# Optimization experiments

Hardware: AMD Instinct MI355X
Metric: run time of the kernel (lower is better)

## Reference

```python
import jax, jax.numpy as jnp
import numpy as np

B, N_CHANS, T = 128, 64, 1000
SPATIAL_EXP, SPATIAL_MERGE = 240, 32
FILTERS = [41, 51, 61]
TEMP_EXP = 2
BASE = 2
FEATURE_DIM = [(SPATIAL_EXP // (N_CHANS - BASE**i + 1), BASE**i)
               for i in range(2, 6) if BASE**i < N_CHANS] + [(SPATIAL_EXP, N_CHANS)]
SUM_SP = sum(d0 * (N_CHANS - d1 + 1) for d0, d1 in FEATURE_DIM)   # 1078
N_FEAT = len(FILTERS) * TEMP_EXP * SPATIAL_MERGE                  # 192
FC_IN = (N_FEAT + 1) * N_FEAT // 2                                # 18528
N_CLASS = 4
BN_EPS = 1e-5


def _conv2d(x, w, b, groups=1, pad_w=0):
    y = jax.lax.conv_general_dilated(
        x, w, (1, 1), ((0, 0), (pad_w, pad_w)),
        dimension_numbers=('NCHW', 'OIHW', 'NCHW'),
        feature_group_count=groups)
    return y + b[None, :, None, None]


def _bn(x, gamma, beta):
    # inference-mode BatchNorm2d with running_mean=0, running_var=1
    return gamma[None, :, None, None] * x * (1.0 / np.sqrt(1.0 + BN_EPS)) + beta[None, :, None, None]


def setup_inputs() -> dict:
    key = jax.random.key(0)
    ks = iter(jax.random.split(key, 40))
    inp = {"x": jax.random.normal(next(ks), (B, N_CHANS, T), jnp.float32)}
    for i, (d0, d1) in enumerate(FEATURE_DIM):
        inp[f"sw{i}"] = jax.random.normal(next(ks), (d0, 1, d1, 1), jnp.float32) / np.sqrt(d1)
        inp[f"sb{i}"] = jnp.zeros((d0,), jnp.float32)
    inp["mw"] = jax.random.normal(next(ks), (SPATIAL_MERGE, 1, SUM_SP, 1), jnp.float32) / np.sqrt(SUM_SP)
    inp["mb"] = jnp.zeros((SPATIAL_MERGE,), jnp.float32)
    inp["mg"] = jnp.ones((SPATIAL_MERGE,), jnp.float32)
    inp["mbt"] = jnp.zeros((SPATIAL_MERGE,), jnp.float32)
    for i, size in enumerate(FILTERS):
        co = TEMP_EXP * SPATIAL_MERGE
        inp[f"tw{i}"] = jax.random.normal(next(ks), (co, 1, 1, size), jnp.float32) / np.sqrt(size)
        inp[f"tb{i}"] = jnp.zeros((co,), jnp.float32)
        inp[f"tg{i}"] = jnp.ones((co,), jnp.float32)
        inp[f"tbt{i}"] = jnp.zeros((co,), jnp.float32)
    inp["fcw"] = jax.random.normal(next(ks), (N_CLASS, FC_IN), jnp.float32) / np.sqrt(FC_IN)
    inp["fcb"] = jnp.zeros((N_CLASS,), jnp.float32)
    return inp


def reference(x, sw0, sb0, sw1, sb1, sw2, sb2, sw3, sb3, sw4, sb4,
              mw, mb, mg, mbt,
              tw0, tb0, tg0, tbt0, tw1, tb1, tg1, tbt1, tw2, tb2, tg2, tbt2,
              fcw, fcb):
    b, _, t = x.shape
    xi = x[:, None]                                        # (B,1,C,T)
    sp = [(sw0, sb0), (sw1, sb1), (sw2, sb2), (sw3, sb3), (sw4, sb4)]
    feats = [_conv2d(xi, w, bb).reshape(b, -1, t) for w, bb in sp]
    Xs = jnp.concatenate(feats, 1)[:, None]                # (B,1,1078,T)
    Xs = _bn(_conv2d(Xs, mw, mb), mg, mbt)                 # (B,32,1,T)
    tp = [(tw0, tb0, tg0, tbt0), (tw1, tb1, tg1, tbt1), (tw2, tb2, tg2, tbt2)]
    Xt = jnp.stack([_bn(_conv2d(Xs, w, bb, groups=SPATIAL_MERGE, pad_w=w.shape[-1] // 2), g, bt)
                    for w, bb, g, bt in tp], 1)            # (B,3,64,1,T)
    Xt = Xt.reshape(b, -1, t)                              # (B,192,T)
    Xb = jnp.einsum('bct,bdt->bcd', Xt, Xt) / (t - 1)      # Gram matrix (B,192,192)
    L = jnp.linalg.cholesky(Xb)
    n = L.shape[-1]
    rows, cols = np.tril_indices(n, -1)                    # row-major: matches torch per-row concat
    diag = jnp.diagonal(L, axis1=1, axis2=2)               # (B,192)
    tangent = jnp.concatenate([jnp.log(diag), L[:, rows, cols]], axis=1)  # (B,18528)
    return tangent @ fcw.T + fcb
```

## Files before the change

### kernel.cpp

```cpp
#include <hip/hip_runtime.h>
#include <hip/hip_bf16.h>
#include <math.h>


#define A_OFF    0
#define BETA_OFF 2048
#define TBE_OFF  2080
#define TWE_OFF  2304
#define XS_OFF   14592
#define XBP_OFF  4110592
#define XT_OFF   7256320
#define WS_NEED  ((size_t)19839232 * 4)

#define SBN 0.9999950000374997f

typedef short short8 __attribute__((ext_vector_type(8)));
typedef float floatx4 __attribute__((ext_vector_type(4)));

__device__ __forceinline__ unsigned short f2bf(float f) {
    unsigned u = __float_as_uint(f);
    u += 0x7FFFu + ((u >> 16) & 1u);
    return (unsigned short)(u >> 16);
}
__device__ __forceinline__ float bf2f(unsigned short h) {
    return __uint_as_float(((unsigned)h) << 16);
}

__global__ __launch_bounds__(256) void prep_kernel(
    const float* __restrict__ sw0, const float* __restrict__ sw1,
    const float* __restrict__ sw2, const float* __restrict__ sw3,
    const float* __restrict__ sw4,
    const float* __restrict__ sb0, const float* __restrict__ sb1,
    const float* __restrict__ sb2, const float* __restrict__ sb3,
    const float* __restrict__ sb4,
    const float* __restrict__ mw, const float* __restrict__ mb,
    const float* __restrict__ mg, const float* __restrict__ mbt,
    const float* __restrict__ tw0, const float* __restrict__ tw1,
    const float* __restrict__ tw2,
    const float* __restrict__ tb0, const float* __restrict__ tb1,
    const float* __restrict__ tb2,
    const float* __restrict__ tg0, const float* __restrict__ tg1,
    const float* __restrict__ tg2,
    const float* __restrict__ tbt0, const float* __restrict__ tbt1,
    const float* __restrict__ tbt2,
    float* __restrict__ ws)
{
    const float* tws[3]  = {tw0, tw1, tw2};
    const float* tbs[3]  = {tb0, tb1, tb2};
    const float* tgs[3]  = {tg0, tg1, tg2};
    const float* tbts[3] = {tbt0, tbt1, tbt2};
    const int fsz[3] = {41, 51, 61};

    int gid = blockIdx.x * 256 + threadIdx.x;
    int gw = gid >> 6, lane = gid & 63;

    if (gw < 2048) {
        int m = gw >> 6, c = gw & 63;
        float acc = 0.f;
        for (int j = lane; j < 1078; j += 64) {
            float wv = mw[m * 1078 + j];
            float sv = 0.f;
            if (j < 183) {
                int r = j, fq = r / 61, h = r - fq * 61, k = c - h;
                if (k >= 0 && k < 4)  sv = sw0[fq * 4 + k];
            } else if (j < 411) {
                int r = j - 183, fq = r / 57, h = r - fq * 57, k = c - h;
                if (k >= 0 && k < 8)  sv = sw1[fq * 8 + k];
            } else if (j < 607) {
                int r = j - 411, fq = r / 49, h = r - fq * 49, k = c - h;
                if (k >= 0 && k < 16) sv = sw2[fq * 16 + k];
            } else if (j < 838) {
                int r = j - 607, fq = r / 33, h = r - fq * 33, k = c - h;
                if (k >= 0 && k < 32) sv = sw3[fq * 32 + k];
            } else {
                int r = j - 838;
                sv = sw4[r * 64 + c];
            }
            acc += wv * sv;
        }
        for (int off = 32; off > 0; off >>= 1) acc += __shfl_down(acc, off);
        if (lane == 0) ws[A_OFF + m * 64 + c] = mg[m] * SBN * acc;
    } else if (gw < 2080) {
        int m = gw - 2048;
        float acc = 0.f;
        for (int j = lane; j < 1078; j += 64) {
            float wv = mw[m * 1078 + j];
            float sv;
            if (j < 183)      sv = sb0[j / 61];
            else if (j < 411) sv = sb1[(j - 183) / 57];
            else if (j < 607) sv = sb2[(j - 411) / 49];
            else if (j < 838) sv = sb3[(j - 607) / 33];
            else              sv = sb4[j - 838];
            acc += wv * sv;
        }
        for (int off = 32; off > 0; off >>= 1) acc += __shfl_down(acc, off);
        if (lane == 0)
            ws[BETA_OFF + m] = mg[m] * SBN * (acc + mb[m]) + mbt[m];
    } else {
        int id2 = gid - 133120;
        if (id2 < 0) return;
        if (id2 < 192) {
            int fi = id2 >> 6, o = id2 & 63;
            ws[TBE_OFF + id2] = tgs[fi][o] * SBN * tbs[fi][o] + tbts[fi][o];
        } else if (id2 < 12480) {
            int idx = id2 - 192;
            int fi = idx >> 12, r = idx & 4095, o = r >> 6, k = r & 63;
            int sz = fsz[fi];
            float v = 0.f;
            if (k < sz) v = tgs[fi][o] * SBN * tws[fi][o * sz + k];
            ws[TWE_OFF + idx] = v;
        }
    }
}

__global__ __launch_bounds__(256) void xs_kernel(const float* __restrict__ x,
                                                 float* __restrict__ ws)
{
    __shared__ float Ash[2048];
    __shared__ float Bsh[32];
    int tid = threadIdx.x;
    for (int i = tid; i < 2048; i += 256) Ash[i] = ws[A_OFF + i];
    if (tid < 32) Bsh[tid] = ws[BETA_OFF + tid];
    __syncthreads();

    int gid = blockIdx.x * 256 + tid;
    int b = gid / 1000, t = gid - b * 1000;
    const float* xp = x + b * 64000 + t;

    float acc[32];
#pragma unroll
    for (int m = 0; m < 32; ++m) acc[m] = Bsh[m];
#pragma unroll 4
    for (int c = 0; c < 64; ++c) {
        float xv = xp[c * 1000];
#pragma unroll
        for (int m = 0; m < 32; ++m) acc[m] += Ash[m * 64 + c] * xv;
    }
    float* op = ws + XS_OFF + b * 32000 + t;
#pragma unroll
    for (int m = 0; m < 32; ++m) op[m * 1000] = acc[m];
}

__device__ __forceinline__ void conv8_vals(float* __restrict__ a,
                                           const float* __restrict__ xp,
                                           const unsigned short* __restrict__ wp,
                                           int szp, float bias)
{
    float xw[8];
#pragma unroll
    for (int i = 0; i < 8; ++i) { a[i] = bias; xw[i] = xp[i]; }
    for (int k = 0; k < szp; k += 8) {
#pragma unroll
        for (int p = 0; p < 8; ++p) {
            float w = bf2f(wp[(k + p) * 64]);
#pragma unroll
            for (int i = 0; i < 8; ++i) a[i] += w * xw[(p + i) & 7];
            xw[p] = xp[k + p + 8];
        }
    }
}

__global__ __launch_bounds__(256) void xt_kernel(float* __restrict__ ws)
{
    __shared__ float xs_sh[32 * 201];
    __shared__ unsigned short tw_sh[10752];
    __shared__ float tb_sh[192];

    int tid = threadIdx.x;
    int wg = blockIdx.x;
    int b = wg >> 3, chunk = wg & 7;
    int t0 = chunk * 128;
    const int fszp[3]  = {48, 56, 64};
    const int fpad[3]  = {20, 25, 30};
    const int twoff[3] = {0, 3072, 6656};

    for (int idx = tid; idx < 10752; idx += 256) {
        int bank, kt, rem;
        if (idx < 3072)      { bank = 0; rem = idx; }
        else if (idx < 6656) { bank = 1; rem = idx - 3072; }
        else                 { bank = 2; rem = idx - 6656; }
        kt = rem >> 6; int o = rem & 63;
        tw_sh[idx] = f2bf(ws[TWE_OFF + bank * 4096 + o * 64 + kt]);
    }
    if (tid < 192) tb_sh[tid] = ws[TBE_OFF + tid];

    const float* xsrow = ws + XS_OFF + b * 32000;
    for (int idx = tid; idx < 6400; idx += 256) {
        int m = idx / 200, q = idx - m * 200;
        int gt = t0 - 30 + q;
        xs_sh[m * 201 + q] = (gt >= 0 && gt < 1000) ? xsrow[m * 1000 + gt] : 0.f;
    }
    __syncthreads();

    unsigned short* xtg = (unsigned short*)(ws + XT_OFF);
    const int lane = tid & 63;
    const int wvid = tid >> 6;
    const int o = lane, m = o >> 1;

#pragma unroll
    for (int it = 0; it < 3; ++it) {
        int g = it * 4 + wvid;
        int bank = g % 3, tgq = g / 3;
        int ch = bank * 64 + o;
        const unsigned short* wp = &tw_sh[twoff[bank] + o];
        float bias = tb_sh[ch];
        int szp = fszp[bank], base = 30 - fpad[bank];
        unsigned short* op = &xtg[(size_t)(b * 192 + ch) * 1024 + t0 + tgq * 32];
#pragma unroll
        for (int s = 0; s < 4; ++s) {
            int tlb = tgq * 32 + s * 8;
            float a[8];
            conv8_vals(a, &xs_sh[m * 201 + tlb + base], wp, szp, bias);
            short8 hv;
#pragma unroll
            for (int i = 0; i < 8; ++i) {
                int gt = t0 + tlb + i;
                hv[i] = (short)((gt < 1000) ? f2bf(a[i]) : 0);
            }
            *(short8*)&op[s * 8] = hv;
        }
    }
}

__global__ __launch_bounds__(256) void gram_kernel(float* __restrict__ ws)
{
    __shared__ __align__(16) unsigned short xsh[192 * 136];

    int tid = threadIdx.x;
    int b = blockIdx.x >> 1, h = blockIdx.x & 1;
    int nrows = h ? 192 : 128;

    const unsigned short* xtg = (const unsigned short*)(ws + XT_OFF);
    const unsigned short* gb = xtg + (size_t)b * 192 * 1024;

    floatx4 acc[3][4];
#pragma unroll
    for (int t = 0; t < 3; ++t)
#pragma unroll
        for (int sj = 0; sj < 4; ++sj) acc[t][sj] = (floatx4){0.f, 0.f, 0.f, 0.f};

    const int lane = tid & 63;
    const int wv   = tid >> 6;
    const int m15  = lane & 15;
    const int quad = lane >> 4;
    int nloads = nrows * 16;

    for (int t0 = 0; t0 < 1024; t0 += 128) {
        for (int idx = tid; idx < nloads; idx += 256) {
            int row = idx >> 4, c8 = idx & 15;
            *(short8*)&xsh[row * 136 + c8 * 8] =
                *(const short8*)&gb[(size_t)row * 1024 + t0 + c8 * 8];
        }
        __syncthreads();
        if (h == 0) {
#pragma unroll
            for (int k0 = 0; k0 < 128; k0 += 32) {
                short8 a0 = *(const short8*)&xsh[(      wv * 16 + m15) * 136 + quad * 8 + k0];
                short8 a1 = *(const short8*)&xsh[( 64 + wv * 16 + m15) * 136 + quad * 8 + k0];
#pragma unroll
                for (int sj = 0; sj < 4; ++sj) {
                    short8 b0 = *(const short8*)&xsh[(      sj * 16 + m15) * 136 + quad * 8 + k0];
                    short8 b1 = *(const short8*)&xsh[( 64 + sj * 16 + m15) * 136 + quad * 8 + k0];
                    acc[0][sj] = __builtin_amdgcn_mfma_f32_16x16x32_bf16(a0, b0, acc[0][sj], 0, 0, 0);
                    acc[1][sj] = __builtin_amdgcn_mfma_f32_16x16x32_bf16(a1, b0, acc[1][sj], 0, 0, 0);
                    acc[2][sj] = __builtin_amdgcn_mfma_f32_16x16x32_bf16(a1, b1, acc[2][sj], 0, 0, 0);
                }
            }
        } else {
#pragma unroll
            for (int k0 = 0; k0 < 128; k0 += 32) {
                short8 a2 = *(const short8*)&xsh[(128 + wv * 16 + m15) * 136 + quad * 8 + k0];
#pragma unroll
                for (int sj = 0; sj < 4; ++sj) {
                    short8 b0 = *(const short8*)&xsh[(      sj * 16 + m15) * 136 + quad * 8 + k0];
                    short8 b1 = *(const short8*)&xsh[( 64 + sj * 16 + m15) * 136 + quad * 8 + k0];
                    short8 b2 = *(const short8*)&xsh[(128 + sj * 16 + m15) * 136 + quad * 8 + k0];
                    acc[0][sj] = __builtin_amdgcn_mfma_f32_16x16x32_bf16(a2, b0, acc[0][sj], 0, 0, 0);
                    acc[1][sj] = __builtin_amdgcn_mfma_f32_16x16x32_bf16(a2, b1, acc[1][sj], 0, 0, 0);
                    acc[2][sj] = __builtin_amdgcn_mfma_f32_16x16x32_bf16(a2, b2, acc[2][sj], 0, 0, 0);
                }
            }
        }
        __syncthreads();
    }

    const float sc = 1.0f / 999.0f;
#pragma unroll
    for (int t = 0; t < 3; ++t) {
        int tileid = h ? (3 + t) : t;
        float* xbp = ws + XBP_OFF + b * 24576 + tileid * 4096;
#pragma unroll
        for (int sj = 0; sj < 4; ++sj)
#pragma unroll
            for (int r = 0; r < 4; ++r) {
                int i = wv * 16 + quad * 4 + r;
                int j = sj * 16 + m15;
                xbp[i * 64 + j] = acc[t][sj][r] * sc;
            }
    }
}

__global__ __launch_bounds__(256, 3) void cov_kernel(float* __restrict__ ws)
{
    __shared__ float xs_sh[32 * 129];
    __shared__ __align__(16) unsigned short xt_sh[2 * 64 * 72];
    __shared__ unsigned short tw_sh[120 * 64];
    __shared__ float tb_sh[128];

    int tid = threadIdx.x;
    int wg = blockIdx.x;
    int b = wg / 6, tile = wg - b * 6;
    const int TIa[6] = {0, 1, 1, 2, 2, 2};
    const int TJa[6] = {0, 0, 1, 0, 1, 2};
    int I = TIa[tile], J = TJa[tile];
    const int fpad[3] = {20, 25, 30};
    const int fszp[3] = {48, 56, 64};
    int padI = fpad[I], szpI = fszp[I];
    int padJ = fpad[J], szpJ = fszp[J];
    bool diag = (I == J);

    int nI = szpI * 64;
    for (int idx = tid; idx < nI; idx += 256) {
        int kt = idx >> 6, o = idx & 63;
        tw_sh[idx] = f2bf(ws[TWE_OFF + I * 4096 + o * 64 + kt]);
    }
    if (!diag) {
        int nJ = szpJ * 64;
        for (int idx = tid; idx < nJ; idx += 256) {
            int kt = idx >> 6, o = idx & 63;
            tw_sh[nI + idx] = f2bf(ws[TWE_OFF + J * 4096 + o * 64 + kt]);
        }
    }
    if (tid < 64)        tb_sh[tid] = ws[TBE_OFF + I * 64 + tid];
    else if (tid < 128)  tb_sh[tid] = ws[TBE_OFF + J * 64 + (tid - 64)];

    floatx4 acc[4];
#pragma unroll
    for (int sj = 0; sj < 4; ++sj) acc[sj] = (floatx4){0.f, 0.f, 0.f, 0.f};

    const float* xsrow = ws + XS_OFF + b * 32000;
    unsigned short* xtI = xt_sh;
    unsigned short* xtJ = diag ? xt_sh : (xt_sh + 64 * 72);

    const int lane = tid & 63;
    const int wv   = tid >> 6;
    const int m15  = lane & 15;
    const int quad = lane >> 4;

    for (int t0 = 0; t0 < 1000; t0 += 64) {
        for (int idx = tid; idx < 4096; idx += 256) {
            int m = idx >> 7, q = idx & 127;
            int gt = t0 - 30 + q;
            xs_sh[m * 129 + q] = (gt >= 0 && gt < 1000) ? xsrow[m * 1000 + gt] : 0.f;
        }
        __syncthreads();
        for (int it = 0; it < 2; ++it) {
            int o   = lane;
            int grp = wv + it * 4;
            int tlb = grp * 8;
            int m   = o >> 1;
            float a[8];
            conv8_vals(a, &xs_sh[m * 129 + tlb + (30 - padI)], &tw_sh[o],
                       szpI, tb_sh[o]);
            short8 hv;
#pragma unroll
            for (int i = 0; i < 8; ++i) {
                int gt = t0 + tlb + i;
                hv[i] = (short)((gt < 1000) ? f2bf(a[i]) : 0);
            }
            *(short8*)&xtI[o * 72 + tlb] = hv;
            if (!diag) {
                conv8_vals(a, &xs_sh[m * 129 + tlb + (30 - padJ)], &tw_sh[nI + o],
                           szpJ, tb_sh[64 + o]);
#pragma unroll
                for (int i = 0; i < 8; ++i) {
                    int gt = t0 + tlb + i;
                    hv[i] = (short)((gt < 1000) ? f2bf(a[i]) : 0);
                }
                *(short8*)&xtJ[o * 72 + tlb] = hv;
            }
        }
        __syncthreads();
        const unsigned short* ap = &xtI[(wv * 16 + m15) * 72 + quad * 8];
#pragma unroll
        for (int k0 = 0; k0 < 64; k0 += 32) {
            short8 af = *(const short8*)(ap + k0);
#pragma unroll
            for (int sj = 0; sj < 4; ++sj) {
                short8 bf = *(const short8*)&xtJ[(sj * 16 + m15) * 72 + quad * 8 + k0];
                acc[sj] = __builtin_amdgcn_mfma_f32_16x16x32_bf16(af, bf, acc[sj],
                                                                  0, 0, 0);
            }
        }
        __syncthreads();
    }

    float* xbp = ws + XBP_OFF + b * 24576 + tile * 4096;
    const float sc = 1.0f / 999.0f;
#pragma unroll
    for (int sj = 0; sj < 4; ++sj)
#pragma unroll
        for (int r = 0; r < 4; ++r) {
            int i = wv * 16 + quad * 4 + r;
            int j = sj * 16 + m15;
            xbp[i * 64 + j] = acc[sj][r] * sc;
        }
}

#define LSTR 196
__device__ __forceinline__ int lidx(int i, int c) {
    return i * LSTR + ((((c >> 2) ^ ((i >> 3) & 7)) << 2) | (c & 3));
}

__device__ __forceinline__ void diag16(float* Lm, int j0, int i,
                                       float* invd_sh)
{
    float r[16];
#pragma unroll
    for (int c = 0; c < 16; ++c) r[c] = Lm[lidx(j0 + i, j0 + c)];
#pragma unroll
    for (int jj = 0; jj < 16; ++jj) {
        float d = __shfl(r[jj], jj);
        d = fmaxf(d, 1e-20f);
        float s = sqrtf(d);
        float inv = 1.0f / s;
        if (i == jj) { r[jj] = s; invd_sh[jj] = inv; }
        else if (i > jj) r[jj] *= inv;
#pragma unroll
        for (int cc = jj + 1; cc < 16; ++cc) {
            float vc = __shfl(r[jj], cc);
            if (i >= cc) r[cc] -= r[jj] * vc;
        }
    }
#pragma unroll
    for (int c = 0; c < 16; ++c)
        if (c <= i) Lm[lidx(j0 + i, j0 + c)] = r[c];
}

__global__ __launch_bounds__(512) void chol_kernel(const float* __restrict__ ws,
                                                   const float* __restrict__ fcw,
                                                   const float* __restrict__ fcb,
                                                   float* __restrict__ out)
{
    __shared__ __align__(16) float L[192 * LSTR];
    __shared__ float invd_sh[16];
    __shared__ float red[8][4];

    int b = blockIdx.x, tid = threadIdx.x;
    const float* Xb = ws + XBP_OFF + b * 24576;
    const int TIa[6] = {0, 1, 1, 2, 2, 2};
    const int TJa[6] = {0, 0, 1, 0, 1, 2};

    for (int idx = tid; idx < 6144; idx += 512) {
        int fi = idx << 2;
        int t = fi >> 12, r = (fi >> 6) & 63, c = fi & 63;
        floatx4 val = *(const floatx4*)&Xb[fi];
        *(floatx4*)&L[lidx(TIa[t] * 64 + r, TJa[t] * 64 + c)] = val;
    }
    __syncthreads();

    if (tid < 16) diag16(L, 0, tid, invd_sh);
    __syncthreads();

    for (int p = 0; p <= 10; ++p) {
        int j0 = p * 16, j1 = j0 + 16;

        {
            int i = j1 + tid;
            if (i < 192) {
                floatx4 vv[4];
#pragma unroll
                for (int q = 0; q < 4; ++q)
                    vv[q] = *(floatx4*)&L[lidx(i, j0 + 4 * q)];
                float v[16];
#pragma unroll
                for (int k = 0; k < 16; ++k) v[k] = vv[k >> 2][k & 3];
#pragma unroll
                for (int k = 0; k < 16; ++k) {
                    float vk = v[k];
#pragma unroll
                    for (int p2 = 0; p2 < k; ++p2)
                        vk -= v[p2] * L[lidx(j0 + k, j0 + p2)];
                    v[k] = vk * invd_sh[k];
                }
#pragma unroll
                for (int k = 0; k < 16; ++k) vv[k >> 2][k & 3] = v[k];
#pragma unroll
                for (int q = 0; q < 4; ++q)
                    *(floatx4*)&L[lidx(i, j0 + 4 * q)] = vv[q];
            }
        }
        __syncthreads();

        int RT = (192 - j1) >> 3;
        int nt = RT * RT + RT;
        if (tid < 64) {
            int r = tid & 15, cq = tid >> 4;
            floatx4 a4 = *(floatx4*)&L[lidx(j1 + r, j1 + cq * 4)];
#pragma unroll
            for (int k = 0; k < 16; ++k) {
                float pr = L[lidx(j1 + r, j0 + k)];
#pragma unroll
                for (int cc = 0; cc < 4; ++cc)
                    a4[cc] -= pr * L[lidx(j1 + cq * 4 + cc, j0 + k)];
            }
            *(floatx4*)&L[lidx(j1 + r, j1 + cq * 4)] = a4;
            if (tid < 16) diag16(L, j1, tid, invd_sh);
        } else {
            for (int t = 6 + (tid - 64); t < nt; t += 448) {
                int ti = (int)(sqrtf((float)t + 0.25f) - 0.5f);
                while (ti * ti + ti > t) --ti;
                while ((ti + 1) * (ti + 1) + (ti + 1) <= t) ++ti;
                int tj = t - ti * ti - ti;
                int i0 = j1 + 8 * ti, c0 = j1 + 4 * tj;
                floatx4 a[8];
#pragma unroll
                for (int r = 0; r < 8; ++r)
                    a[r] = *(floatx4*)&L[lidx(i0 + r, c0)];
#pragma unroll 1
                for (int kk = 0; kk < 16; kk += 4) {
                    floatx4 pi[8], pc[4];
#pragma unroll
                    for (int r = 0; r < 8; ++r)
                        pi[r] = *(floatx4*)&L[lidx(i0 + r, j0 + kk)];
#pragma unroll
                    for (int c = 0; c < 4; ++c)
                        pc[c] = *(floatx4*)&L[lidx(c0 + c, j0 + kk)];
#pragma unroll
                    for (int k = 0; k < 4; ++k)
#pragma unroll
                        for (int r = 0; r < 8; ++r) {
                            float ar = pi[r][k];
#pragma unroll
                            for (int c = 0; c < 4; ++c)
                                a[r][c] -= ar * pc[c][k];
                        }
                }
#pragma unroll
                for (int r = 0; r < 8; ++r)
                    *(floatx4*)&L[lidx(i0 + r, c0)] = a[r];
            }
        }
        __syncthreads();
    }

    float a0 = 0.f, a1 = 0.f, a2 = 0.f, a3 = 0.f;
    for (int d = tid; d < 192; d += 512) {
        float v = logf(fmaxf(L[lidx(d, d)], 1e-30f));
        a0 += v * fcw[d];
        a1 += v * fcw[18528 + d];
        a2 += v * fcw[2 * 18528 + d];
        a3 += v * fcw[3 * 18528 + d];
    }
    {
        int e = tid;
        float fe = (float)e;
        int r = (int)((1.0f + sqrtf(1.0f + 8.0f * fe)) * 0.5f);
        if (r < 1) r = 1;
        while (r * (r - 1) / 2 > e) --r;
        while ((r + 1) * r / 2 <= e) ++r;
        int c = e - r * (r - 1) / 2;
        for (; e < 18336; e += 512) {
            float v = L[lidx(r, c)];
            int dd = 192 + e;
            a0 += v * fcw[dd];
            a1 += v * fcw[18528 + dd];
            a2 += v * fcw[2 * 18528 + dd];
            a3 += v * fcw[3 * 18528 + dd];
            c += 512;
            while (c >= r) { c -= r; ++r; }
        }
    }
    for (int off = 32; off > 0; off >>= 1) {
        a0 += __shfl_down(a0, off);
        a1 += __shfl_down(a1, off);
        a2 += __shfl_down(a2, off);
        a3 += __shfl_down(a3, off);
    }
    int wv = tid >> 6, ln = tid & 63;
    if (ln == 0) { red[wv][0] = a0; red[wv][1] = a1; red[wv][2] = a2; red[wv][3] = a3; }
    __syncthreads();
    if (tid < 4) {
        float s = red[0][tid] + red[1][tid] + red[2][tid] + red[3][tid]
                + red[4][tid] + red[5][tid] + red[6][tid] + red[7][tid]
                + fcb[tid];
        out[b * 4 + tid] = s;
    }
}

extern "C" void kernel_launch(void* const* d_in, const int* in_sizes, int n_in,
                              void* d_out, int out_size, void* d_ws, size_t ws_size,
                              hipStream_t stream)
{
    float* ws = (float*)d_ws;

    prep_kernel<<<569, 256, 0, stream>>>(
        (const float*)d_in[1], (const float*)d_in[3], (const float*)d_in[5],
        (const float*)d_in[7], (const float*)d_in[9],
        (const float*)d_in[2], (const float*)d_in[4], (const float*)d_in[6],
        (const float*)d_in[8], (const float*)d_in[10],
        (const float*)d_in[11], (const float*)d_in[12], (const float*)d_in[13],
        (const float*)d_in[14],
        (const float*)d_in[15], (const float*)d_in[19], (const float*)d_in[23],
        (const float*)d_in[16], (const float*)d_in[20], (const float*)d_in[24],
        (const float*)d_in[17], (const float*)d_in[21], (const float*)d_in[25],
        (const float*)d_in[18], (const float*)d_in[22], (const float*)d_in[26], ws);
    xs_kernel<<<500, 256, 0, stream>>>((const float*)d_in[0], ws);
    if (ws_size >= WS_NEED) {
        xt_kernel<<<1024, 256, 0, stream>>>(ws);
        gram_kernel<<<256, 256, 0, stream>>>(ws);
    } else {
        cov_kernel<<<768, 256, 0, stream>>>(ws);
    }
    chol_kernel<<<128, 512, 0, stream>>>(ws, (const float*)d_in[27],
                                         (const float*)d_in[28], (float*)d_out);
}
```

Baseline: 355.7 us.

## Restructure temporal conv kernel: register-resident weights, 16-wide outputs, 384 threads

The temporal depthwise conv kernel now uses 6 waves per block, one per (filter bank, time half), instead of 4 waves each looping over three tasks. Each thread keeps its bf16 filter taps, packed in pairs, in registers loaded from shared memory, and computes 16 outputs per sliding window instead of 8. Filter sizes are template parameters so loops fully unroll. This cuts shared-memory weight reads and loop overhead per FMA, at the cost of higher register pressure, which may lower occupancy.

```diff
diff --git a/kernel.cpp b/kernel.cpp
--- a/kernel.cpp
+++ b/kernel.cpp
@@ -160,32 +160,82 @@
     }
 }
 
-__global__ __launch_bounds__(256) void xt_kernel(float* __restrict__ ws)
+template<int SZP>
+__device__ __forceinline__ void conv16(float* __restrict__ a,
+                                       const float* __restrict__ xp,
+                                       const unsigned int* __restrict__ w2,
+                                       float bias)
+{
+    float xw[16];
+#pragma unroll
+    for (int i = 0; i < 16; ++i) { a[i] = bias; xw[i] = xp[i]; }
+#pragma unroll
+    for (int k = 0; k < SZP; k += 8) {
+#pragma unroll
+        for (int p = 0; p < 8; ++p) {
+            unsigned int u = w2[(k + p) >> 1];
+            float w = ((p & 1) == 0) ? __uint_as_float(u << 16)
+                                     : __uint_as_float(u & 0xffff0000u);
+#pragma unroll
+            for (int i = 0; i < 16; ++i)
+                a[i] += w * xw[(k + p + i) & 15];
+            xw[(k + p) & 15] = xp[k + p + 16];
+        }
+    }
+}
+
+template<int SZP, int BASE>
+__device__ __forceinline__ void xt_task(const float* __restrict__ xp0,
+                                        const unsigned int* __restrict__ w2s,
+                                        int o, float bias,
+                                        unsigned short* __restrict__ op,
+                                        int tbase)
+{
+    unsigned int w2[SZP / 2];
+#pragma unroll
+    for (int j = 0; j < SZP / 2; ++j) w2[j] = w2s[j * 64 + o];
+#pragma unroll
+    for (int s = 0; s < 4; ++s) {
+        float a[16];
+        conv16<SZP>(a, xp0 + s * 16 + BASE, w2, bias);
+#pragma unroll
+        for (int half = 0; half < 2; ++half) {
+            short8 hv;
+#pragma unroll
+            for (int i = 0; i < 8; ++i) {
+                int gt = tbase + s * 16 + half * 8 + i;
+                hv[i] = (short)((gt < 1000) ? f2bf(a[half * 8 + i]) : 0);
+            }
+            *(short8*)&op[s * 16 + half * 8] = hv;
+        }
+    }
+}
+
+__global__ __launch_bounds__(384) void xt_kernel(float* __restrict__ ws)
 {
     __shared__ float xs_sh[32 * 201];
-    __shared__ unsigned short tw_sh[10752];
+    __shared__ unsigned int tw2_sh[5376];
     __shared__ float tb_sh[192];
 
     int tid = threadIdx.x;
     int wg = blockIdx.x;
     int b = wg >> 3, chunk = wg & 7;
     int t0 = chunk * 128;
-    const int fszp[3]  = {48, 56, 64};
-    const int fpad[3]  = {20, 25, 30};
-    const int twoff[3] = {0, 3072, 6656};
-
-    for (int idx = tid; idx < 10752; idx += 256) {
-        int bank, kt, rem;
-        if (idx < 3072)      { bank = 0; rem = idx; }
-        else if (idx < 6656) { bank = 1; rem = idx - 3072; }
-        else                 { bank = 2; rem = idx - 6656; }
-        kt = rem >> 6; int o = rem & 63;
-        tw_sh[idx] = f2bf(ws[TWE_OFF + bank * 4096 + o * 64 + kt]);
+
+    for (int idx = tid; idx < 5376; idx += 384) {
+        int bank, rem;
+        if (idx < 1536)      { bank = 0; rem = idx; }
+        else if (idx < 3328) { bank = 1; rem = idx - 1536; }
+        else                 { bank = 2; rem = idx - 3328; }
+        int kt2 = rem >> 6, o = rem & 63;
+        unsigned int lo = f2bf(ws[TWE_OFF + bank * 4096 + o * 64 + 2 * kt2]);
+        unsigned int hi = f2bf(ws[TWE_OFF + bank * 4096 + o * 64 + 2 * kt2 + 1]);
+        tw2_sh[idx] = lo | (hi << 16);
     }
     if (tid < 192) tb_sh[tid] = ws[TBE_OFF + tid];
 
     const float* xsrow = ws + XS_OFF + b * 32000;
-    for (int idx = tid; idx < 6400; idx += 256) {
+    for (int idx = tid; idx < 6400; idx += 384) {
         int m = idx / 200, q = idx - m * 200;
         int gt = t0 - 30 + q;
         xs_sh[m * 201 + q] = (gt >= 0 && gt < 1000) ? xsrow[m * 1000 + gt] : 0.f;
@@ -194,32 +244,18 @@
 
     unsigned short* xtg = (unsigned short*)(ws + XT_OFF);
     const int lane = tid & 63;
-    const int wvid = tid >> 6;
+    const int wv   = tid >> 6;
+    const int bank = wv % 3, thalf = wv / 3;
     const int o = lane, m = o >> 1;
-
-#pragma unroll
-    for (int it = 0; it < 3; ++it) {
-        int g = it * 4 + wvid;
-        int bank = g % 3, tgq = g / 3;
-        int ch = bank * 64 + o;
-        const unsigned short* wp = &tw_sh[twoff[bank] + o];
-        float bias = tb_sh[ch];
-        int szp = fszp[bank], base = 30 - fpad[bank];
-        unsigned short* op = &xtg[(size_t)(b * 192 + ch) * 1024 + t0 + tgq * 32];
-#pragma unroll
-        for (int s = 0; s < 4; ++s) {
-            int tlb = tgq * 32 + s * 8;
-            float a[8];
-            conv8_vals(a, &xs_sh[m * 201 + tlb + base], wp, szp, bias);
-            short8 hv;
-#pragma unroll
-            for (int i = 0; i < 8; ++i) {
-                int gt = t0 + tlb + i;
-                hv[i] = (short)((gt < 1000) ? f2bf(a[i]) : 0);
-            }
-            *(short8*)&op[s * 8] = hv;
-        }
-    }
+    const int ch = bank * 64 + o;
+    float bias = tb_sh[ch];
+    int tbase = t0 + thalf * 64;
+    unsigned short* op = &xtg[(size_t)(b * 192 + ch) * 1024 + tbase];
+    const float* xp0 = &xs_sh[m * 201 + thalf * 64];
+
+    if (bank == 0)      xt_task<48, 10>(xp0, &tw2_sh[0],    o, bias, op, tbase);
+    else if (bank == 1) xt_task<56, 5>( xp0, &tw2_sh[1536], o, bias, op, tbase);
+    else                xt_task<64, 0>( xp0, &tw2_sh[3328], o, bias, op, tbase);
 }
 
 __global__ __launch_bounds__(256) void gram_kernel(float* __restrict__ ws)
@@ -607,7 +643,7 @@
         (const float*)d_in[18], (const float*)d_in[22], (const float*)d_in[26], ws);
     xs_kernel<<<500, 256, 0, stream>>>((const float*)d_in[0], ws);
     if (ws_size >= WS_NEED) {
-        xt_kernel<<<1024, 256, 0, stream>>>(ws);
+        xt_kernel<<<1024, 384, 0, stream>>>(ws);
         gram_kernel<<<256, 256, 0, stream>>>(ws);
     } else {
         cov_kernel<<<768, 256, 0, stream>>>(ws);
```

Measured after the change: 508.1 us. 1.43x slower.
